# Optimization experiments

Measured on AMD Instinct MI355X. Metric: run time of the kernel, lower is better.

## Reference

```python
import jax, jax.numpy as jnp
import numpy as np

KNN_K = 8
WINDOW = 3  # temporal_window + 1 candidate frames
LN_EPS = 1e-5
NORM_EPS = 1e-12


def setup_inputs() -> dict:
    key = jax.random.key(0)
    B, T, M, D, H = 2, 8, 512, 1024, 1024
    ks = jax.random.split(key, 12)
    s = 0.02
    return {
        "z": jax.random.normal(ks[0], (B, T, M, D), jnp.float32),
        "Wq": jax.random.normal(ks[1], (D, D), jnp.float32) * s,
        "Wv": jax.random.normal(ks[2], (D, D), jnp.float32) * s,
        "Wout": jax.random.normal(ks[3], (D, D), jnp.float32) * s,
        "ln_w": jnp.ones((D,), jnp.float32),
        "ln_b": jnp.zeros((D,), jnp.float32),
        "Watt_q": jax.random.normal(ks[4], (D, D), jnp.float32) * s,
        "Watt_k": jax.random.normal(ks[5], (D, D), jnp.float32) * s,
        "W_ih": jax.random.normal(ks[6], (3 * H, D), jnp.float32) * s,
        "W_hh": jax.random.normal(ks[7], (3 * H, H), jnp.float32) * s,
        "b_ih": jnp.zeros((3 * H,), jnp.float32),
        "b_hh": jnp.zeros((3 * H,), jnp.float32),
        "W_mf": jax.random.normal(ks[8], (D, H), jnp.float32) * s,
        "b_mf": jnp.zeros((D,), jnp.float32),
    }


def _forward(z, Wq, Wv, Wout, ln_w, ln_b, Watt_q, Watt_k,
             W_ih, W_hh, b_ih, b_hh, W_mf, b_mf):
    B, T, M, D = z.shape
    H = W_hh.shape[1]
    # cosine normalization (torch F.normalize with eps clamp)
    zn = z / jnp.maximum(jnp.linalg.norm(z, axis=-1, keepdims=True), NORM_EPS)
    mem = jnp.zeros((B, M, H), z.dtype)
    b_ar = jnp.arange(B)[:, None, None]
    outs = []
    for t in range(T):  # T is static; fully vectorized over B, M, k inside
        tts = t - jnp.arange(WINDOW)          # candidate frames t, t-1, t-2
        valid = tts >= 0                      # [W]
        cand = zn[:, jnp.clip(tts, 0)]        # [B,W,M,D]
        # cosine similarity query nodes at t vs all candidates (dt-major order)
        sim = jnp.einsum('bmd,bwnd->bmwn', zn[:, t], cand).reshape(B, M, WINDOW * M)
        sim = jnp.where(jnp.repeat(valid, M)[None, None, :], sim, -jnp.inf)
        vals, idx = jax.lax.top_k(sim, KNN_K)  # [B,M,k]
        dt = idx // M
        j = idx % M
        tt = jnp.clip(t - dt, 0)
        Kfeat = z[b_ar, tt, j]                 # [B,M,k,D] gathered neighbors
        # GAT quirk faithful to source: scalar logit scale from node 0's query,
        # first output coordinate only, shared across all nodes of (b,t)
        s0 = z[:, t, 0] @ Watt_q[0]            # [B]
        kh_sum = (Kfeat @ Watt_k.T).sum(-1)    # [B,M,k]
        att = jax.nn.softmax(s0[:, None, None] * kh_sum, axis=-1)
        alpha = 0.5 * vals + 0.5 * att         # [B,M,k]
        msg = jnp.einsum('bmk,bmkd->bmd', alpha, Kfeat @ Wv.T)
        h_t = z[:, t]                          # [B,M,D]
        x = msg + h_t @ Wq.T
        mu = x.mean(-1, keepdims=True)
        var = ((x - mu) ** 2).mean(-1, keepdims=True)
        x = (x - mu) / jnp.sqrt(var + LN_EPS) * ln_w + ln_b
        inp = x @ Wout.T
        # torch GRUCell: gates ordered (r, z, n)
        gi = inp @ W_ih.T + b_ih               # [B,M,3H]
        gh = mem @ W_hh.T + b_hh
        ir, iz, inn = jnp.split(gi, 3, axis=-1)
        hr, hz, hn = jnp.split(gh, 3, axis=-1)
        r = jax.nn.sigmoid(ir + hr)
        zg = jax.nn.sigmoid(iz + hz)
        n = jnp.tanh(inn + r * hn)
        mem = (1.0 - zg) * n + zg * mem
        outs.append(h_t + mem @ W_mf.T + b_mf)
    h = jnp.stack(outs, axis=1)                # [B,T,M,D]
    return h, mem


def reference(z, Wq, Wv, Wout, ln_w, ln_b, Watt_q, Watt_k,
              W_ih, W_hh, b_ih, b_hh, W_mf, b_mf):
    return _forward(z, Wq, Wv, Wout, ln_w, ln_b, Watt_q, Watt_k,
                    W_ih, W_hh, b_ih, b_hh, W_mf, b_mf)
```

## Files before the change

### kernel.cpp

```cpp
#include <hip/hip_runtime.h>
#include <hip/hip_bf16.h>
#include <math.h>

#define B_ 2
#define T_ 8
#define M_ 512
#define D_ 1024
#define H_ 1024
#define NC_ 1536
#define KNN 8

typedef __hip_bfloat16 bf16;
typedef short v8s __attribute__((ext_vector_type(8)));
typedef float v4f __attribute__((ext_vector_type(4)));

__device__ __forceinline__ float b2f(short s) {
  union { unsigned u; float f; } x; x.u = ((unsigned)(unsigned short)s) << 16; return x.f;
}
__device__ __forceinline__ short f2b(float f) {
  bf16 h = __float2bfloat16(f); return *(short*)&h;
}

__device__ __forceinline__ void async16(const void* g, void* l) {
  __builtin_amdgcn_global_load_lds(
      (const __attribute__((address_space(1))) void*)g,
      (__attribute__((address_space(3))) void*)l, 16, 0, 0);
}

__device__ __forceinline__ void mfma_loop(const bf16* __restrict__ A,
                                          const bf16* __restrict__ Bp,
                                          int K, v4f (&acc)[4][4],
                                          bf16* sA, bf16* sB)
{
  const int tid  = threadIdx.x;
  const int lane = tid & 63;
  const int wave = tid >> 6;
  const int quad = lane >> 4;
  const int l15  = lane & 15;
  const int wr = (wave >> 1) * 64;
  const int wc = (wave & 1) * 64;

  const int r0 = tid >> 2, g0 = (tid & 3) ^ ((r0 >> 1) & 3);
  const int c1 = tid + 256;
  const int r1 = c1 >> 2,  g1 = (c1 & 3) ^ ((r1 >> 1) & 3);

  const bf16* a0p = A  + (size_t)r0*K + g0*8;
  const bf16* a1p = A  + (size_t)r1*K + g1*8;
  const bf16* b0p = Bp + (size_t)r0*K + g0*8;
  const bf16* b1p = Bp + (size_t)r1*K + g1*8;
  bf16* la0 = sA + tid*8;  bf16* la1 = sA + c1*8;
  bf16* lb0 = sB + tid*8;  bf16* lb1 = sB + c1*8;

  int aoff[4], boff[4];
  #pragma unroll
  for (int i = 0; i < 4; ++i) {
    int ra = wr + i*16 + l15;
    aoff[i] = (ra*4 + (quad ^ ((ra >> 1) & 3))) * 8;
    int rb = wc + i*16 + l15;
    boff[i] = (rb*4 + (quad ^ ((rb >> 1) & 3))) * 8;
  }

  for (int k0 = 0; k0 < K; k0 += 32) {
    __syncthreads();
    async16(a0p + k0, la0);
    async16(a1p + k0, la1);
    async16(b0p + k0, lb0);
    async16(b1p + k0, lb1);
    __syncthreads();
    v8s af[4], bfr[4];
    #pragma unroll
    for (int i = 0; i < 4; ++i) af[i]  = *(const v8s*)(sA + aoff[i]);
    #pragma unroll
    for (int i = 0; i < 4; ++i) bfr[i] = *(const v8s*)(sB + boff[i]);
    #pragma unroll
    for (int mi = 0; mi < 4; ++mi)
      #pragma unroll
      for (int ni = 0; ni < 4; ++ni)
        acc[mi][ni] = __builtin_amdgcn_mfma_f32_16x16x32_bf16(
            af[mi], bfr[ni], acc[mi][ni], 0, 0, 0);
  }
}

__device__ __forceinline__ void out_tile(int oid, int tp,
    const bf16* __restrict__ memhb, const bf16* __restrict__ Wmfb,
    const float* __restrict__ b_mf, const float* __restrict__ z,
    float* __restrict__ out, bf16* sA, bf16* sB)
{
  const int rb = oid >> 3, cb = oid & 7;
  const int g0 = (rb >> 2)*4096 + tp*512 + (rb & 3)*128;
  v4f acc[4][4];
  #pragma unroll
  for (int i = 0; i < 4; ++i)
    #pragma unroll
    for (int j = 0; j < 4; ++j) acc[i][j] = (v4f){0.f,0.f,0.f,0.f};
  mfma_loop(memhb + (size_t)g0*H_, Wmfb + (size_t)(cb*128)*H_, H_, acc, sA, sB);
  const int tid = threadIdx.x, lane = tid & 63, wave = tid >> 6;
  const int quad = lane >> 4, l15 = lane & 15;
  const int wr = (wave >> 1) * 64, wcc = (wave & 1) * 64;
  #pragma unroll
  for (int ni = 0; ni < 4; ++ni) {
    const int col = cb*128 + wcc + ni*16 + l15;
    const float bv = b_mf[col];
    #pragma unroll
    for (int mi = 0; mi < 4; ++mi) {
      const int rowb = g0 + wr + mi*16 + quad*4;
      #pragma unroll
      for (int reg = 0; reg < 4; ++reg) {
        const int row = rowb + reg;
        out[(size_t)row*D_ + col] = acc[mi][ni][reg] + bv + z[(size_t)row*D_ + col];
      }
    }
  }
}

template<bool DUAL, bool STATS>
__global__ __launch_bounds__(256) void k_bgemm(
    const bf16* __restrict__ A1, const bf16* __restrict__ B1,
    const bf16* __restrict__ A2, const bf16* __restrict__ B2,
    bf16* __restrict__ Cv, int N, int K,
    float* __restrict__ ssum, float* __restrict__ ssq)
{
  __shared__ bf16 sA[128*32];
  __shared__ bf16 sB[128*32];
  v4f acc[4][4];
  #pragma unroll
  for (int i = 0; i < 4; ++i)
    #pragma unroll
    for (int j = 0; j < 4; ++j) acc[i][j] = (v4f){0.f,0.f,0.f,0.f};

  const int row0 = blockIdx.y * 128, col0 = blockIdx.x * 128;
  mfma_loop(A1 + (size_t)row0*K, B1 + (size_t)col0*K, K, acc, sA, sB);
  if constexpr (DUAL)
    mfma_loop(A2 + (size_t)row0*K, B2 + (size_t)col0*K, K, acc, sA, sB);

  const int tid = threadIdx.x, lane = tid & 63, wave = tid >> 6;
  const int quad = lane >> 4, l15 = lane & 15;
  const int wr = (wave >> 1) * 64, wc = (wave & 1) * 64;

  float st_s[4][4], st_q[4][4];
  if constexpr (STATS) {
    #pragma unroll
    for (int a = 0; a < 4; ++a)
      #pragma unroll
      for (int b = 0; b < 4; ++b) { st_s[a][b] = 0.f; st_q[a][b] = 0.f; }
  }

  #pragma unroll
  for (int ni = 0; ni < 4; ++ni) {
    const int col = col0 + wc + ni*16 + l15;
    #pragma unroll
    for (int mi = 0; mi < 4; ++mi) {
      const int rowb = row0 + wr + mi*16 + quad*4;
      #pragma unroll
      for (int reg = 0; reg < 4; ++reg) {
        float v = acc[mi][ni][reg];
        if constexpr (STATS) { st_s[mi][reg] += v; st_q[mi][reg] += v*v; }
        Cv[(size_t)(rowb+reg)*N + col] = __float2bfloat16(v);
      }
    }
  }

  if constexpr (STATS) {
    const int p = blockIdx.x*2 + (wave & 1);
    #pragma unroll
    for (int mi = 0; mi < 4; ++mi)
      #pragma unroll
      for (int reg = 0; reg < 4; ++reg) {
        float s = st_s[mi][reg], q = st_q[mi][reg];
        #pragma unroll
        for (int o = 1; o < 16; o <<= 1) {
          s += __shfl_xor(s, o, 64);
          q += __shfl_xor(q, o, 64);
        }
        if (l15 == 0) {
          const int row = row0 + wr + mi*16 + quad*4 + reg;
          ssum[(size_t)p*8192 + row] = s;
          ssq [(size_t)p*8192 + row] = q;
        }
      }
  }
}

__global__ __launch_bounds__(256) void k_gic(
    const bf16* __restrict__ Xb, const bf16* __restrict__ Wcb,
    const float* __restrict__ ssum, const float* __restrict__ ssq,
    const float* __restrict__ u2, const float* __restrict__ v2b,
    bf16* __restrict__ Cv)
{
  __shared__ bf16 sA[128*32];
  __shared__ bf16 sB[128*32];
  __shared__ float smu[128], srs[128];
  const int row0 = blockIdx.y * 128, col0 = blockIdx.x * 128;
  const int tid = threadIdx.x;
  if (tid < 128) {
    int r = row0 + tid;
    float s = 0.f, q = 0.f;
    #pragma unroll
    for (int p = 0; p < 16; ++p) { s += ssum[(size_t)p*8192 + r]; q += ssq[(size_t)p*8192 + r]; }
    float mu = s * (1.f/D_);
    float var = q * (1.f/D_) - mu*mu;
    smu[tid] = mu; srs[tid] = rsqrtf(var + 1e-5f);
  }
  __syncthreads();

  v4f acc[4][4];
  #pragma unroll
  for (int i = 0; i < 4; ++i)
    #pragma unroll
    for (int j = 0; j < 4; ++j) acc[i][j] = (v4f){0.f,0.f,0.f,0.f};
  mfma_loop(Xb + (size_t)row0*D_, Wcb + (size_t)col0*D_, D_, acc, sA, sB);

  const int lane = tid & 63, wave = tid >> 6;
  const int quad = lane >> 4, l15 = lane & 15;
  const int wr = (wave >> 1) * 64, wc = (wave & 1) * 64;
  #pragma unroll
  for (int ni = 0; ni < 4; ++ni) {
    const int col = col0 + wc + ni*16 + l15;
    const float uj = u2[col], vj = v2b[col];
    #pragma unroll
    for (int mi = 0; mi < 4; ++mi) {
      const int rl = wr + mi*16 + quad*4;
      #pragma unroll
      for (int reg = 0; reg < 4; ++reg) {
        const float mu = smu[rl+reg], rs = srs[rl+reg];
        float v = rs*acc[mi][ni][reg] - mu*rs*uj + vj;
        Cv[(size_t)(row0+rl+reg)*(3*H_) + col] = __float2bfloat16(v);
      }
    }
  }
}

__global__ __launch_bounds__(256) void k_sims(const bf16* __restrict__ znhi,
                                              const bf16* __restrict__ znlo,
                                              const float* __restrict__ z,
                                              const float* __restrict__ wks,
                                              float* __restrict__ sim,
                                              float* __restrict__ kh,
                                              const bf16* __restrict__ Wihb,
                                              const bf16* __restrict__ WoutTb,
                                              const float* __restrict__ u,
                                              const float* __restrict__ vv,
                                              const float* __restrict__ b_ih,
                                              bf16* __restrict__ Wcb,
                                              float* __restrict__ u2,
                                              float* __restrict__ v2b)
{
  __shared__ bf16 sAh[128*32];
  __shared__ bf16 sAl[128*32];
  __shared__ bf16 sBh[128*32];
  __shared__ bf16 sBl[128*32];

  const int zi = blockIdx.z;
  const int tid  = threadIdx.x;
  const int lane = tid & 63;
  const int wave = tid >> 6;

  if (zi >= 176) {
    const int slot = (zi - 176)*16 + blockIdx.y*4 + blockIdx.x;
    if (slot < 192) {
      const int yc = slot >> 3, xc = slot & 7;
      v4f acc[4][4];
      #pragma unroll
      for (int i = 0; i < 4; ++i)
        #pragma unroll
        for (int j = 0; j < 4; ++j) acc[i][j] = (v4f){0.f,0.f,0.f,0.f};
      mfma_loop(Wihb + (size_t)(yc*128)*D_, WoutTb + (size_t)(xc*128)*D_,
                D_, acc, sAh, sBh);
      const int quad = lane >> 4, l15 = lane & 15;
      const int wr = (wave >> 1) * 64, wcc = (wave & 1) * 64;
      #pragma unroll
      for (int ni = 0; ni < 4; ++ni) {
        const int col = xc*128 + wcc + ni*16 + l15;
        #pragma unroll
        for (int mi = 0; mi < 4; ++mi) {
          const int rowb = yc*128 + wr + mi*16 + quad*4;
          #pragma unroll
          for (int reg = 0; reg < 4; ++reg)
            Wcb[(size_t)(rowb+reg)*D_ + col] = __float2bfloat16(acc[mi][ni][reg]);
        }
      }
    } else {
      int g = (slot - 192)*256 + tid;
      if (g < 3*H_) {
        const bf16* wr_ = Wihb + (size_t)g*D_;
        float du = 0.f, dv = 0.f;
        for (int k = 0; k < 128; ++k) {
          v8s wv = *(const v8s*)(wr_ + k*8);
          #pragma unroll
          for (int e = 0; e < 8; ++e) {
            float wf = b2f(wv[e]);
            du += wf * u[k*8+e];
            dv += wf * vv[k*8+e];
          }
        }
        u2[g] = du; v2b[g] = dv + b_ih[g];
      }
    }
    return;
  }

  if (zi >= 48) {
    int kid = (zi - 48)*16 + blockIdx.y*4 + blockIdx.x;
    int r = kid*4 + wave;
    const float* zp = z + (size_t)r*D_ + lane*16;
    const float* wp = wks + lane*16;
    float p = 0.f;
    #pragma unroll
    for (int j = 0; j < 4; ++j) {
      float4 a = *(const float4*)(zp + j*4);
      float4 b = *(const float4*)(wp + j*4);
      p += a.x*b.x + a.y*b.y + a.z*b.z + a.w*b.w;
    }
    for (int o = 32; o; o >>= 1) p += __shfl_down(p, o, 64);
    if (lane == 0) kh[r] = p;
    return;
  }

  const int w  = zi % 3;
  const int bt = zi / 3;
  const int b  = bt / T_;
  const int t  = bt % T_;
  if (w > t) return;
  if (w == 0 && blockIdx.y > blockIdx.x) return;
  const int tw = t - w;
  const int arow0 = bt*M_ + blockIdx.y*128;
  const int brow0 = (b*T_ + tw)*M_ + blockIdx.x*128;

  const bf16* Ah = znhi + (size_t)arow0*D_;
  const bf16* Al = znlo + (size_t)arow0*D_;
  const bf16* Bh = znhi + (size_t)brow0*D_;
  const bf16* Bl = znlo + (size_t)brow0*D_;

  v4f acc[4][4];
  #pragma unroll
  for (int i = 0; i < 4; ++i)
    #pragma unroll
    for (int j = 0; j < 4; ++j) acc[i][j] = (v4f){0.f,0.f,0.f,0.f};

  const int quad = lane >> 4;
  const int l15  = lane & 15;
  const int wr = (wave >> 1) * 64;
  const int wc = (wave & 1) * 64;

  const int r0 = tid >> 2, g0 = (tid & 3) ^ ((r0 >> 1) & 3);
  const int c1 = tid + 256;
  const int r1 = c1 >> 2,  g1 = (c1 & 3) ^ ((r1 >> 1) & 3);
  const size_t o0 = (size_t)r0*D_ + g0*8;
  const size_t o1 = (size_t)r1*D_ + g1*8;

  int aoff[4], boff[4];
  #pragma unroll
  for (int i = 0; i < 4; ++i) {
    int ra = wr + i*16 + l15;
    aoff[i] = (ra*4 + (quad ^ ((ra >> 1) & 3))) * 8;
    int rb = wc + i*16 + l15;
    boff[i] = (rb*4 + (quad ^ ((rb >> 1) & 3))) * 8;
  }

  for (int k0 = 0; k0 < D_; k0 += 32) {
    __syncthreads();
    async16(Ah + o0 + k0, sAh + tid*8);
    async16(Ah + o1 + k0, sAh + c1*8);
    async16(Al + o0 + k0, sAl + tid*8);
    async16(Al + o1 + k0, sAl + c1*8);
    async16(Bh + o0 + k0, sBh + tid*8);
    async16(Bh + o1 + k0, sBh + c1*8);
    async16(Bl + o0 + k0, sBl + tid*8);
    async16(Bl + o1 + k0, sBl + c1*8);
    __syncthreads();
    v8s ah[4], al[4], bh[4], bl[4];
    #pragma unroll
    for (int i = 0; i < 4; ++i) {
      ah[i] = *(const v8s*)(sAh + aoff[i]);
      al[i] = *(const v8s*)(sAl + aoff[i]);
      bh[i] = *(const v8s*)(sBh + boff[i]);
      bl[i] = *(const v8s*)(sBl + boff[i]);
    }
    #pragma unroll
    for (int mi = 0; mi < 4; ++mi)
      #pragma unroll
      for (int ni = 0; ni < 4; ++ni) {
        acc[mi][ni] = __builtin_amdgcn_mfma_f32_16x16x32_bf16(ah[mi], bh[ni], acc[mi][ni], 0, 0, 0);
        acc[mi][ni] = __builtin_amdgcn_mfma_f32_16x16x32_bf16(ah[mi], bl[ni], acc[mi][ni], 0, 0, 0);
        acc[mi][ni] = __builtin_amdgcn_mfma_f32_16x16x32_bf16(al[mi], bh[ni], acc[mi][ni], 0, 0, 0);
      }
  }

  float* C = sim + (size_t)bt*M_*NC_;
  const int rowbase = blockIdx.y*128 + wr;
  const int colbase = w*M_ + blockIdx.x*128 + wc;
  const bool mir = (w == 0) && (blockIdx.y != blockIdx.x);
  #pragma unroll
  for (int ni = 0; ni < 4; ++ni) {
    const int col = colbase + ni*16 + l15;
    #pragma unroll
    for (int mi = 0; mi < 4; ++mi) {
      const int rowb = rowbase + mi*16 + quad*4;
      #pragma unroll
      for (int reg = 0; reg < 4; ++reg)
        C[(size_t)(rowb+reg)*NC_ + col] = acc[mi][ni][reg];
      if (mir)
        *(float4*)(C + (size_t)col*NC_ + rowb) = *(float4*)&acc[mi][ni];
    }
  }
}

__global__ __launch_bounds__(256) void k_fgru2(
    const bf16* __restrict__ membIn, const bf16* __restrict__ Whhb,
    const bf16* __restrict__ gib, const float* __restrict__ b_hh,
    float* __restrict__ mem, bf16* __restrict__ membOut,
    bf16* __restrict__ memhb, float* __restrict__ outT,
    const bf16* __restrict__ Wmfb, const float* __restrict__ b_mf,
    const float* __restrict__ z, float* __restrict__ outMain, int t)
{
  __shared__ bf16 smem[8192];

  if (blockIdx.y >= 16) {
    out_tile((blockIdx.y-16)*16 + blockIdx.x, t-1,
             memhb, Wmfb, b_mf, z, outMain, smem, smem + 4096);
    return;
  }

  bf16* sA = smem;
  const int row0 = blockIdx.y*64, col0 = blockIdx.x*64;

  const int tid  = threadIdx.x;
  const int lane = tid & 63;
  const int wave = tid >> 6;
  const int quad = lane >> 4;
  const int l15  = lane & 15;
  const int wr   = (wave >> 1) * 32;
  const int wcol = (wave & 1) * 32;

  const int rA = tid >> 2, gA = (tid & 3) ^ ((rA >> 1) & 3);
  const size_t aofs = (size_t)rA*H_ + gA*8;
  const size_t bofs = (size_t)(col0 + rA)*H_ + gA*8;

  int aoff[2], boff[2];
  #pragma unroll
  for (int i = 0; i < 2; ++i) {
    int ra = wr + i*16 + l15;
    aoff[i] = (ra*4 + (quad ^ ((ra >> 1) & 3))) * 8;
    int rb = wcol + i*16 + l15;
    boff[i] = (rb*4 + (quad ^ ((rb >> 1) & 3))) * 8;
  }

  v4f acc[3][2][2];
  #pragma unroll
  for (int g = 0; g < 3; ++g)
    #pragma unroll
    for (int i = 0; i < 2; ++i)
      #pragma unroll
      for (int j = 0; j < 2; ++j) acc[g][i][j] = (v4f){0.f,0.f,0.f,0.f};

  if (t > 0) {
    const bf16* prev = membIn + (size_t)row0*H_;
    for (int k0 = 0; k0 < H_; k0 += 32) {
      __syncthreads();
      async16(prev + aofs + k0, sA + tid*8);
      async16(Whhb + bofs + k0,           smem + 2048 + tid*8);
      async16(Whhb + 1048576 + bofs + k0, smem + 4096 + tid*8);
      async16(Whhb + 2097152 + bofs + k0, smem + 6144 + tid*8);
      __syncthreads();
      v8s af[2], bfr[3][2];
      #pragma unroll
      for (int i = 0; i < 2; ++i) af[i] = *(const v8s*)(sA + aoff[i]);
      #pragma unroll
      for (int g = 0; g < 3; ++g)
        #pragma unroll
        for (int i = 0; i < 2; ++i)
          bfr[g][i] = *(const v8s*)(smem + 2048 + g*2048 + boff[i]);
      #pragma unroll
      for (int g = 0; g < 3; ++g)
        #pragma unroll
        for (int mi = 0; mi < 2; ++mi)
          #pragma unroll
          for (int ni = 0; ni < 2; ++ni)
            acc[g][mi][ni] = __builtin_amdgcn_mfma_f32_16x16x32_bf16(
                af[mi], bfr[g][ni], acc[g][mi][ni], 0, 0, 0);
    }
  }

  #pragma unroll
  for (int ni = 0; ni < 2; ++ni) {
    const int col = col0 + wcol + ni*16 + l15;
    const float bhr = b_hh[col];
    const float bhz = b_hh[H_ + col];
    const float bhn = b_hh[2*H_ + col];
    #pragma unroll
    for (int mi = 0; mi < 2; ++mi) {
      const int rowb = row0 + wr + mi*16 + quad*4;
      #pragma unroll
      for (int reg = 0; reg < 4; ++reg) {
        const int row = rowb + reg;
        const int b = row >> 9, m = row & 511;
        const size_t btm = (size_t)((b*T_ + t)*M_ + m);
        const bf16* gp = gib + btm*(3*H_);
        float ir  = b2f(*(const short*)(gp + col));
        float iz  = b2f(*(const short*)(gp + H_ + col));
        float inn = b2f(*(const short*)(gp + 2*H_ + col));
        float hr = acc[0][mi][ni][reg] + bhr;
        float hz = acc[1][mi][ni][reg] + bhz;
        float hn = acc[2][mi][ni][reg] + bhn;
        float rgt = 1.f/(1.f + expf(-(ir + hr)));
        float zgt = 1.f/(1.f + expf(-(iz + hz)));
        float n   = tanhf(inn + rgt*hn);
        const size_t mo = (size_t)row*H_ + col;
        float mold = (t > 0) ? mem[mo] : 0.f;
        float mnew = (1.f - zgt)*n + zgt*mold;
        mem[mo] = mnew;
        bf16 mb = __float2bfloat16(mnew);
        membOut[mo] = mb;
        memhb[btm*H_ + col] = mb;
        if (t == T_-1) outT[mo] = mnew;
      }
    }
  }
}

__global__ __launch_bounds__(256) void k_outtail(
    const bf16* __restrict__ memhb, const bf16* __restrict__ Wmfb,
    const float* __restrict__ b_mf, const float* __restrict__ z,
    float* __restrict__ outMain)
{
  __shared__ bf16 smem[8192];
  out_tile(blockIdx.y*8 + blockIdx.x, T_-1, memhb, Wmfb, b_mf, z, outMain,
           smem, smem + 4096);
}

__global__ __launch_bounds__(256) void k_prep(
    const float* __restrict__ Wq, const float* __restrict__ Wv,
    const float* __restrict__ Wout, const float* __restrict__ Wih,
    const float* __restrict__ Whh, const float* __restrict__ Wmf,
    const float* __restrict__ lnw, const float* __restrict__ lnb,
    const float* __restrict__ Wattk, const float* __restrict__ Wattq,
    const float* __restrict__ z,
    bf16* __restrict__ Wdst, float* __restrict__ wks,
    float* __restrict__ u, float* __restrict__ vv, float* __restrict__ s0,
    bf16* __restrict__ zb, bf16* __restrict__ znhi, bf16* __restrict__ znlo,
    bf16* __restrict__ WoutTb)
{
  __shared__ float ps[4], pk[4];
  __shared__ bf16 tr[128*130];
  const int bid = blockIdx.x, tid = threadIdx.x;

  if (bid < 10240) {
    int i = bid*256 + tid;
    const float* src; int base;
    if      (i <  262144) { src = Wq;   base = 0; }
    else if (i <  524288) { src = Wv;   base = 262144; }
    else if (i <  786432) { src = Wout; base = 524288; }
    else if (i < 1572864) { src = Wih;  base = 786432; }
    else if (i < 2359296) { src = Whh;  base = 1572864; }
    else                  { src = Wmf;  base = 2359296; }
    float4 v = ((const float4*)src)[i - base];
    *(short4*)(Wdst + (size_t)i*4) = make_short4(f2b(v.x), f2b(v.y), f2b(v.z), f2b(v.w));
  } else if (bid < 10368) {
    int rc = bid - 10240;
    int rowc = rc >> 2, colc = rc & 3;
    int d = colc*256 + tid;
    float s = 0.f;
    for (int r = rowc*32; r < rowc*32 + 32; ++r) s += Wattk[(size_t)r*D_ + d];
    atomicAdd(&wks[d], s);
  } else if (bid < 10624) {
    int j = (bid - 10368)*4 + (tid >> 6);
    int l = tid & 63;
    const float* wr_ = Wout + (size_t)j*D_ + l*16;
    const float* aw = lnw + l*16;
    const float* ab = lnb + l*16;
    float pu = 0.f, pv = 0.f;
    #pragma unroll
    for (int q = 0; q < 4; ++q) {
      float4 a = *(const float4*)(wr_ + q*4);
      float4 x = *(const float4*)(aw + q*4);
      float4 y = *(const float4*)(ab + q*4);
      pu += a.x*x.x + a.y*x.y + a.z*x.z + a.w*x.w;
      pv += a.x*y.x + a.y*y.y + a.z*y.z + a.w*y.w;
    }
    for (int o = 32; o; o >>= 1) { pu += __shfl_down(pu, o, 64); pv += __shfl_down(pv, o, 64); }
    if (l == 0) { u[j] = pu; vv[j] = pv; }
  } else if (bid < 10640) {
    int bt = bid - 10624;
    int d = tid*4;
    float4 a = *(const float4*)(z + (size_t)bt*M_*D_ + d);
    float4 q = *(const float4*)(Wattq + d);
    float p = a.x*q.x + a.y*q.y + a.z*q.z + a.w*q.w;
    for (int o = 32; o; o >>= 1) p += __shfl_down(p, o, 64);
    if ((tid & 63) == 0) ps[tid >> 6] = p;
    __syncthreads();
    if (tid == 0) s0[bt] = ps[0]+ps[1]+ps[2]+ps[3];
  } else if (bid < 18832) {
    int row = bid - 10640;
    const float* zr = z + (size_t)row*D_;
    int d = tid*4;
    float4 v = *(const float4*)(zr + d);
    float ss = v.x*v.x + v.y*v.y + v.z*v.z + v.w*v.w;
    for (int o = 32; o; o >>= 1) ss += __shfl_down(ss, o, 64);
    if ((tid & 63) == 0) pk[tid >> 6] = ss;
    __syncthreads();
    float s = pk[0]+pk[1]+pk[2]+pk[3];
    float rn = 1.0f / fmaxf(sqrtf(s), 1e-12f);
    *(short4*)(zb + (size_t)row*D_ + d) = make_short4(f2b(v.x), f2b(v.y), f2b(v.z), f2b(v.w));
    float zn[4] = {v.x*rn, v.y*rn, v.z*rn, v.w*rn};
    short hi[4], lo[4];
    #pragma unroll
    for (int j = 0; j < 4; ++j) {
      hi[j] = f2b(zn[j]);
      lo[j] = f2b(zn[j] - b2f(hi[j]));
    }
    *(short4*)(znhi + (size_t)row*D_ + d) = make_short4(hi[0],hi[1],hi[2],hi[3]);
    *(short4*)(znlo + (size_t)row*D_ + d) = make_short4(lo[0],lo[1],lo[2],lo[3]);
  } else {
    int idx = bid - 18832;
    int bi = idx >> 3, bd = idx & 7;
    int c4 = tid & 31, rr = tid >> 5;
    float4 lw4 = *(const float4*)(lnw + bd*128 + c4*4);
    #pragma unroll 4
    for (int it = 0; it < 16; ++it) {
      int i = it*8 + rr;
      float4 v = *(const float4*)(Wout + (size_t)(bi*128+i)*D_ + bd*128 + c4*4);
      int d0 = c4*4;
      tr[(d0+0)*130 + i] = __float2bfloat16(v.x*lw4.x);
      tr[(d0+1)*130 + i] = __float2bfloat16(v.y*lw4.y);
      tr[(d0+2)*130 + i] = __float2bfloat16(v.z*lw4.z);
      tr[(d0+3)*130 + i] = __float2bfloat16(v.w*lw4.w);
    }
    __syncthreads();
    #pragma unroll 4
    for (int it = 0; it < 16; ++it) {
      int d = it*8 + rr;
      short4 o;
      o.x = *(short*)&tr[d*130 + c4*4+0];
      o.y = *(short*)&tr[d*130 + c4*4+1];
      o.z = *(short*)&tr[d*130 + c4*4+2];
      o.w = *(short*)&tr[d*130 + c4*4+3];
      *(short4*)(WoutTb + (size_t)(bd*128+d)*D_ + bi*128 + c4*4) = o;
    }
  }
}

__global__ __launch_bounds__(256) void k_topk(
    const float* __restrict__ sim, const float* __restrict__ kh,
    const float* __restrict__ s0, const bf16* __restrict__ zb,
    bf16* __restrict__ kbarb)
{
  const int wave = threadIdx.x >> 6, l = threadIdx.x & 63;
  const int r  = blockIdx.x*4 + wave;
  const int bt = r >> 9, m = r & 511;
  const int b  = bt >> 3, t = bt & 7;
  const float* srow = sim + (size_t)bt*M_*NC_ + (size_t)m*NC_;
  const int limit = (t >= 2) ? NC_ : ((t == 1) ? 2*M_ : M_);

  float v[24];
  #pragma unroll
  for (int j = 0; j < 24; ++j) {
    int i = j*64 + l;
    v[j] = (i < limit) ? srow[i] : -INFINITY;
  }

  float selv[KNN]; int seli[KNN];
  #pragma unroll
  for (int k = 0; k < KNN; ++k) {
    float bv = v[0]; int bj = 0;
    #pragma unroll
    for (int j = 1; j < 24; ++j)
      if (v[j] > bv) { bv = v[j]; bj = j; }
    int bi = bj*64 + l;
    #pragma unroll
    for (int o = 1; o < 64; o <<= 1) {
      float ov = __shfl_xor(bv, o, 64);
      int   oi = __shfl_xor(bi, o, 64);
      if (ov > bv || (ov == bv && oi < bi)) { bv = ov; bi = oi; }
    }
    selv[k] = bv; seli[k] = bi;
    if ((bi & 63) == l) {
      int jj = bi >> 6;
      #pragma unroll
      for (int j = 0; j < 24; ++j) if (j == jj) v[j] = -INFINITY;
    }
  }

  float khv = 0.f;
  if (l < KNN) {
    int idx = seli[l];
    int w = idx >> 9, n = idx & 511;
    int tt = t - w;
    khv = kh[(b*T_ + tt)*M_ + n];
  }
  float s0v = s0[bt];
  float att[KNN], mx = -INFINITY;
  #pragma unroll
  for (int k = 0; k < KNN; ++k) { att[k] = s0v * __shfl(khv, k, 64); mx = fmaxf(mx, att[k]); }
  float den = 0.f;
  #pragma unroll
  for (int k = 0; k < KNN; ++k) { att[k] = expf(att[k]-mx); den += att[k]; }
  float rden = 1.0f/den;
  float alpha[KNN];
  #pragma unroll
  for (int k = 0; k < KNN; ++k) alpha[k] = 0.5f*selv[k] + 0.5f*att[k]*rden;

  const int d0 = l*16;
  float o[16];
  #pragma unroll
  for (int e = 0; e < 16; ++e) o[e] = 0.f;
  #pragma unroll
  for (int k = 0; k < KNN; ++k) {
    int idx = seli[k];
    int w = idx >> 9, n = idx & 511;
    int tt = t - w;
    const bf16* zp = zb + ((size_t)((b*T_ + tt)*M_ + n))*D_ + d0;
    v8s z0 = *(const v8s*)zp;
    v8s z1 = *(const v8s*)(zp + 8);
    float al = alpha[k];
    #pragma unroll
    for (int e = 0; e < 8; ++e) {
      o[e]   = fmaf(al, b2f(z0[e]), o[e]);
      o[8+e] = fmaf(al, b2f(z1[e]), o[8+e]);
    }
  }
  bf16* kp = kbarb + (size_t)r*D_ + d0;
  short outv[16];
  #pragma unroll
  for (int e = 0; e < 16; ++e) outv[e] = f2b(o[e]);
  *(v8s*)kp       = *(v8s*)outv;
  *(v8s*)(kp + 8) = *(v8s*)(outv + 8);
}

extern "C" void kernel_launch(void* const* d_in, const int* in_sizes, int n_in,
                              void* d_out, int out_size, void* d_ws, size_t ws_size,
                              hipStream_t stream) {
  (void)in_sizes; (void)n_in; (void)out_size; (void)ws_size;
  const float* z      = (const float*)d_in[0];
  const float* Wq     = (const float*)d_in[1];
  const float* Wv     = (const float*)d_in[2];
  const float* Wout   = (const float*)d_in[3];
  const float* ln_w   = (const float*)d_in[4];
  const float* ln_b   = (const float*)d_in[5];
  const float* Watt_q = (const float*)d_in[6];
  const float* Watt_k = (const float*)d_in[7];
  const float* W_ih   = (const float*)d_in[8];
  const float* W_hh   = (const float*)d_in[9];
  const float* b_ih   = (const float*)d_in[10];
  const float* b_hh   = (const float*)d_in[11];
  const float* W_mf   = (const float*)d_in[12];
  const float* b_mf   = (const float*)d_in[13];
  float* out = (float*)d_out;
  float* ws  = (float*)d_ws;

  float* sim   = ws;
  bf16*  GIb   = (bf16*)ws;
  bf16*  znhi  = (bf16*)(ws + 12582912);
  bf16*  Xb    = znhi;
  bf16*  zb    = (bf16*)(ws + 16777216);
  bf16*  kbarb = (bf16*)(ws + 20971520);
  bf16*  memhb = (bf16*)(ws + 25165824);
  bf16*  znlo  = memhb;
  bf16*  mA    = (bf16*)(ws + 29360128);
  bf16*  mB    = (bf16*)(ws + 29884416);
  float* mem   = ws + 30408704;
  bf16*  Wqb   = (bf16*)(ws + 31457280);
  bf16*  Wvb   = Wqb + 1048576;
  bf16*  Wihb  = Wqb + 3145728;
  bf16*  Whhb  = Wqb + 6291456;
  bf16*  Wmfb  = Wqb + 9437184;
  float* wks   = ws + 36700160;
  float* s0    = ws + 36701184;
  float* kh    = ws + 36701200;
  float* u     = ws + 36709392;
  float* vv    = ws + 36710416;
  float* ssum  = ws + 36711440;
  float* ssq   = ws + 36842512;
  float* u2    = ws + 36973584;
  float* v2b   = ws + 36976656;
  bf16*  Wcb   = (bf16*)(ws + 36979728);
  bf16*  WoutTb= (bf16*)(ws + 38552592);

  hipMemsetAsync(wks, 0, 1024*sizeof(float), stream);

  k_prep<<<dim3(18896), dim3(256), 0, stream>>>(
      Wq, Wv, Wout, W_ih, W_hh, W_mf, ln_w, ln_b, Watt_k, Watt_q, z,
      Wqb, wks, u, vv, s0, zb, znhi, znlo, WoutTb);

  k_sims<<<dim3(4,4,189), dim3(256), 0, stream>>>(
      znhi, znlo, z, wks, sim, kh,
      Wihb, WoutTb, u, vv, b_ih, Wcb, u2, v2b);

  k_topk<<<dim3(2048), dim3(256), 0, stream>>>(sim, kh, s0, zb, kbarb);

  k_bgemm<true,true><<<dim3(8,64), dim3(256), 0, stream>>>(
      kbarb, Wvb, zb, Wqb, Xb, D_, D_, ssum, ssq);

  k_gic<<<dim3(24,64), dim3(256), 0, stream>>>(Xb, Wcb, ssum, ssq, u2, v2b, GIb);

  for (int t = 0; t < T_; ++t) {
    bf16*       mout = (t & 1) ? mB : mA;
    const bf16* min_ = (t & 1) ? mA : mB;
    dim3 grid = (t == 0) ? dim3(16,16) : dim3(16,20);
    k_fgru2<<<grid, dim3(256), 0, stream>>>(
        min_, Whhb, GIb, b_hh, mem, mout, memhb,
        out + (size_t)B_*T_*M_*D_, Wmfb, b_mf, z, out, t);
  }

  k_outtail<<<dim3(8,8), dim3(256), 0, stream>>>(memhb, Wmfb, b_mf, z, out);
}
```

Baseline: 679.4 us.

## Move combined-weight GEMM from k_sims into k_topk and drop wks memset

The Wih·WoutT combined-weight GEMM and the u2/v2b matvec blocks move out of the k_sims grid and into extra leading blocks of k_topk, so they run alongside the memory-bound top-k work instead of lengthening the sims GEMM tail. The Watt_k column-sum is rewritten so four blocks each sum all rows directly, which removes the atomics and the separate hipMemsetAsync. In exchange, those four blocks each loop over 1024 rows serially, which may lengthen the prep kernel's tail, and k_topk's LDS use grows.

```diff
diff --git a/kernel.cpp b/kernel.cpp
--- a/kernel.cpp
+++ b/kernel.cpp
@@ -235,15 +235,7 @@
                                               const float* __restrict__ z,
                                               const float* __restrict__ wks,
                                               float* __restrict__ sim,
-                                              float* __restrict__ kh,
-                                              const bf16* __restrict__ Wihb,
-                                              const bf16* __restrict__ WoutTb,
-                                              const float* __restrict__ u,
-                                              const float* __restrict__ vv,
-                                              const float* __restrict__ b_ih,
-                                              bf16* __restrict__ Wcb,
-                                              float* __restrict__ u2,
-                                              float* __restrict__ v2b)
+                                              float* __restrict__ kh)
 {
   __shared__ bf16 sAh[128*32];
   __shared__ bf16 sAl[128*32];
@@ -254,50 +246,6 @@
   const int tid  = threadIdx.x;
   const int lane = tid & 63;
   const int wave = tid >> 6;
-
-  if (zi >= 176) {
-    const int slot = (zi - 176)*16 + blockIdx.y*4 + blockIdx.x;
-    if (slot < 192) {
-      const int yc = slot >> 3, xc = slot & 7;
-      v4f acc[4][4];
-      #pragma unroll
-      for (int i = 0; i < 4; ++i)
-        #pragma unroll
-        for (int j = 0; j < 4; ++j) acc[i][j] = (v4f){0.f,0.f,0.f,0.f};
-      mfma_loop(Wihb + (size_t)(yc*128)*D_, WoutTb + (size_t)(xc*128)*D_,
-                D_, acc, sAh, sBh);
-      const int quad = lane >> 4, l15 = lane & 15;
-      const int wr = (wave >> 1) * 64, wcc = (wave & 1) * 64;
-      #pragma unroll
-      for (int ni = 0; ni < 4; ++ni) {
-        const int col = xc*128 + wcc + ni*16 + l15;
-        #pragma unroll
-        for (int mi = 0; mi < 4; ++mi) {
-          const int rowb = yc*128 + wr + mi*16 + quad*4;
-          #pragma unroll
-          for (int reg = 0; reg < 4; ++reg)
-            Wcb[(size_t)(rowb+reg)*D_ + col] = __float2bfloat16(acc[mi][ni][reg]);
-        }
-      }
-    } else {
-      int g = (slot - 192)*256 + tid;
-      if (g < 3*H_) {
-        const bf16* wr_ = Wihb + (size_t)g*D_;
-        float du = 0.f, dv = 0.f;
-        for (int k = 0; k < 128; ++k) {
-          v8s wv = *(const v8s*)(wr_ + k*8);
-          #pragma unroll
-          for (int e = 0; e < 8; ++e) {
-            float wf = b2f(wv[e]);
-            du += wf * u[k*8+e];
-            dv += wf * vv[k*8+e];
-          }
-        }
-        u2[g] = du; v2b[g] = dv + b_ih[g];
-      }
-    }
-    return;
-  }
 
   if (zi >= 48) {
     int kid = (zi - 48)*16 + blockIdx.y*4 + blockIdx.x;
@@ -556,12 +504,13 @@
     float4 v = ((const float4*)src)[i - base];
     *(short4*)(Wdst + (size_t)i*4) = make_short4(f2b(v.x), f2b(v.y), f2b(v.z), f2b(v.w));
   } else if (bid < 10368) {
-    int rc = bid - 10240;
-    int rowc = rc >> 2, colc = rc & 3;
-    int d = colc*256 + tid;
-    float s = 0.f;
-    for (int r = rowc*32; r < rowc*32 + 32; ++r) s += Wattk[(size_t)r*D_ + d];
-    atomicAdd(&wks[d], s);
+    int c = bid - 10240;
+    if (c < 4) {
+      int d = c*256 + tid;
+      float s = 0.f;
+      for (int r = 0; r < D_; ++r) s += Wattk[(size_t)r*D_ + d];
+      wks[d] = s;
+    }
   } else if (bid < 10624) {
     int j = (bid - 10368)*4 + (tid >> 6);
     int l = tid & 63;
@@ -642,10 +591,61 @@
 __global__ __launch_bounds__(256) void k_topk(
     const float* __restrict__ sim, const float* __restrict__ kh,
     const float* __restrict__ s0, const bf16* __restrict__ zb,
-    bf16* __restrict__ kbarb)
+    bf16* __restrict__ kbarb,
+    const bf16* __restrict__ Wihb, const bf16* __restrict__ WoutTb,
+    const float* __restrict__ u, const float* __restrict__ vv,
+    const float* __restrict__ b_ih,
+    bf16* __restrict__ Wcb, float* __restrict__ u2, float* __restrict__ v2b)
 {
-  const int wave = threadIdx.x >> 6, l = threadIdx.x & 63;
-  const int r  = blockIdx.x*4 + wave;
+  __shared__ bf16 sAB[2*128*32];
+  const int bx = blockIdx.x;
+  const int tid = threadIdx.x;
+
+  if (bx < 192) {
+    const int yc = bx >> 3, xc = bx & 7;
+    v4f acc[4][4];
+    #pragma unroll
+    for (int i = 0; i < 4; ++i)
+      #pragma unroll
+      for (int j = 0; j < 4; ++j) acc[i][j] = (v4f){0.f,0.f,0.f,0.f};
+    mfma_loop(Wihb + (size_t)(yc*128)*D_, WoutTb + (size_t)(xc*128)*D_,
+              D_, acc, sAB, sAB + 4096);
+    const int lane = tid & 63, wave = tid >> 6;
+    const int quad = lane >> 4, l15 = lane & 15;
+    const int wr = (wave >> 1) * 64, wcc = (wave & 1) * 64;
+    #pragma unroll
+    for (int ni = 0; ni < 4; ++ni) {
+      const int col = xc*128 + wcc + ni*16 + l15;
+      #pragma unroll
+      for (int mi = 0; mi < 4; ++mi) {
+        const int rowb = yc*128 + wr + mi*16 + quad*4;
+        #pragma unroll
+        for (int reg = 0; reg < 4; ++reg)
+          Wcb[(size_t)(rowb+reg)*D_ + col] = __float2bfloat16(acc[mi][ni][reg]);
+      }
+    }
+    return;
+  }
+  if (bx < 204) {
+    int g = (bx - 192)*256 + tid;
+    const bf16* wr_ = Wihb + (size_t)g*D_;
+    float du = 0.f, dv = 0.f;
+    for (int k = 0; k < 128; ++k) {
+      v8s wv = *(const v8s*)(wr_ + k*8);
+      #pragma unroll
+      for (int e = 0; e < 8; ++e) {
+        float wf = b2f(wv[e]);
+        du += wf * u[k*8+e];
+        dv += wf * vv[k*8+e];
+      }
+    }
+    u2[g] = du; v2b[g] = dv + b_ih[g];
+    return;
+  }
+  if (bx < 208) return;
+
+  const int wave = tid >> 6, l = tid & 63;
+  const int r  = (bx - 208)*4 + wave;
   const int bt = r >> 9, m = r & 511;
   const int b  = bt >> 3, t = bt & 7;
   const float* srow = sim + (size_t)bt*M_*NC_ + (size_t)m*NC_;
@@ -775,17 +775,15 @@
   bf16*  Wcb   = (bf16*)(ws + 36979728);
   bf16*  WoutTb= (bf16*)(ws + 38552592);
 
-  hipMemsetAsync(wks, 0, 1024*sizeof(float), stream);
-
   k_prep<<<dim3(18896), dim3(256), 0, stream>>>(
       Wq, Wv, Wout, W_ih, W_hh, W_mf, ln_w, ln_b, Watt_k, Watt_q, z,
       Wqb, wks, u, vv, s0, zb, znhi, znlo, WoutTb);
 
-  k_sims<<<dim3(4,4,189), dim3(256), 0, stream>>>(
-      znhi, znlo, z, wks, sim, kh,
+  k_sims<<<dim3(4,4,176), dim3(256), 0, stream>>>(znhi, znlo, z, wks, sim, kh);
+
+  k_topk<<<dim3(2256), dim3(256), 0, stream>>>(
+      sim, kh, s0, zb, kbarb,
       Wihb, WoutTb, u, vv, b_ih, Wcb, u2, v2b);
-
-  k_topk<<<dim3(2048), dim3(256), 0, stream>>>(sim, kh, s0, zb, kbarb);
 
   k_bgemm<true,true><<<dim3(8,64), dim3(256), 0, stream>>>(
       kbarb, Wvb, zb, Wqb, Xb, D_, D_, ssum, ssq);
```

New measurement: 740.6 us. +9.0%, slower.
